# Kernel optimization log

Measured on AMD Instinct MI355X. Metric: run time of the kernel, lower is better.

Reference implementation:

```python
import jax, jax.numpy as jnp
import numpy as np

B, TQ, TP, TC = 8, 8, 447, 1500   # batch, new tokens, past cache len, encoder len
D, H = 1280, 20                   # n_state, n_head
DH = D // H
SCALE = DH ** -0.25               # Whisper scales q and k each by d_head**-0.25
DFF = 4 * D
EPS = 1e-5


def _ln(x, w, b):
    m = jnp.mean(x, axis=-1, keepdims=True)
    v = jnp.mean((x - m) ** 2, axis=-1, keepdims=True)
    return (x - m) * jax.lax.rsqrt(v + EPS) * w + b


def _attn(q, k, v, mask=None):
    # q:[B,Tq,D] k,v:[B,Tk,D]; per-head scaled dot-product attention
    Bq, Tq, _ = q.shape
    Tk = k.shape[1]
    qh = q.reshape(Bq, Tq, H, DH) * SCALE
    kh = k.reshape(Bq, Tk, H, DH) * SCALE
    vh = v.reshape(Bq, Tk, H, DH)
    qk = jnp.einsum('bqhd,bkhd->bhqk', qh, kh)
    if mask is not None:
        qk = qk + mask[None, None, :, :]
    w = jax.nn.softmax(qk, axis=-1)
    return jnp.einsum('bhqk,bkhd->bqhd', w, vh).reshape(Bq, Tq, D)


def setup_inputs() -> dict:
    key = jax.random.key(0)
    ks = jax.random.split(key, 32)
    rn = lambda i, shp, s=1.0: jax.random.normal(ks[i], shp, jnp.float32) * s
    W = 0.02  # weight init scale; weights stored [in,out] so y = x @ W + b
    # additive mask: past fully visible, causal over the TQ new tokens
    i = jnp.arange(TQ)[:, None]
    j = jnp.arange(TQ)[None, :]
    new_mask = jnp.where(j > i, jnp.float32(-1e9), 0.0)
    mask = jnp.concatenate([jnp.zeros((TQ, TP), jnp.float32), new_mask], axis=1)
    return dict(
        x=rn(0, (B, TQ, D)),
        self_k_cache=rn(1, (B, TP, D)),
        self_v_cache=rn(2, (B, TP, D)),
        cross_k=rn(3, (B, TC, D)),
        cross_v=rn(4, (B, TC, D)),
        mask=mask,
        attn_wq=rn(5, (D, D), W), attn_bq=jnp.zeros((D,)),
        attn_wk=rn(6, (D, D), W),                      # Whisper key proj has no bias
        attn_wv=rn(7, (D, D), W), attn_bv=jnp.zeros((D,)),
        attn_wo=rn(8, (D, D), W), attn_bo=jnp.zeros((D,)),
        cross_wq=rn(9, (D, D), W), cross_bq=jnp.zeros((D,)),
        cross_wo=rn(10, (D, D), W), cross_bo=jnp.zeros((D,)),
        attn_ln_w=jnp.ones((D,)), attn_ln_b=jnp.zeros((D,)),
        cross_ln_w=jnp.ones((D,)), cross_ln_b=jnp.zeros((D,)),
        mlp_ln_w=jnp.ones((D,)), mlp_ln_b=jnp.zeros((D,)),
        mlp_w1=rn(11, (D, DFF), W), mlp_b1=jnp.zeros((DFF,)),
        mlp_w2=rn(12, (DFF, D), W), mlp_b2=jnp.zeros((D,)),
        offset=TP,
    )


def reference(x, self_k_cache, self_v_cache, cross_k, cross_v, mask,
              attn_wq, attn_bq, attn_wk, attn_wv, attn_bv, attn_wo, attn_bo,
              cross_wq, cross_bq, cross_wo, cross_bo,
              attn_ln_w, attn_ln_b, cross_ln_w, cross_ln_b, mlp_ln_w, mlp_ln_b,
              mlp_w1, mlp_b1, mlp_w2, mlp_b2, offset):
    # --- self-attention with KV cache ---
    xl = _ln(x, attn_ln_w, attn_ln_b)
    q = xl @ attn_wq + attn_bq
    k1 = xl @ attn_wk
    v1 = xl @ attn_wv + attn_bv
    k = jnp.concatenate([self_k_cache, k1], axis=1)  # [B, TP+TQ, D]
    v = jnp.concatenate([self_v_cache, v1], axis=1)
    x = x + _attn(q, k, v, mask) @ attn_wo + attn_bo
    # --- cross-attention (cross_k/cross_v already projected from encoder) ---
    xl = _ln(x, cross_ln_w, cross_ln_b)
    qc = xl @ cross_wq + cross_bq
    x = x + _attn(qc, cross_k, cross_v) @ cross_wo + cross_bo
    # --- MLP ---
    xl = _ln(x, mlp_ln_w, mlp_ln_b)
    h = jax.nn.gelu(xl @ mlp_w1 + mlp_b1, approximate=False)
    x = x + h @ mlp_w2 + mlp_b2
    return (x, k1, v1)
```

## Files before the change

### kernel.cpp

```cpp
#include <hip/hip_runtime.h>
#include <hip/hip_bf16.h>

#define B_   8
#define TQ_  8
#define TP_  447
#define TC_  1500
#define D_   1280
#define H_   20
#define DH_  64
#define DFF_ 5120
#define M_   64

__global__ __launch_bounds__(256) void ln_kernel(const float* __restrict__ X,
    const float* __restrict__ g, const float* __restrict__ be, float* __restrict__ outT)
{
  __shared__ float redA[4], redB[4];
  const int m = blockIdx.x;
  const int tid = threadIdx.x;
  float v[5];
#pragma unroll
  for (int t = 0; t < 5; ++t) v[t] = X[(size_t)m*D_ + tid + t*256];
  float s = v[0]+v[1]+v[2]+v[3]+v[4];
#pragma unroll
  for (int o = 32; o; o >>= 1) s += __shfl_down(s, o, 64);
  if ((tid & 63) == 0) redA[tid >> 6] = s;
  __syncthreads();
  const float mean = (redA[0]+redA[1]+redA[2]+redA[3]) * (1.0f/D_);
  float q = 0.f;
#pragma unroll
  for (int t = 0; t < 5; ++t) { const float d = v[t]-mean; q += d*d; }
#pragma unroll
  for (int o = 32; o; o >>= 1) q += __shfl_down(q, o, 64);
  if ((tid & 63) == 0) redB[tid >> 6] = q;
  __syncthreads();
  const float rstd = rsqrtf((redB[0]+redB[1]+redB[2]+redB[3]) * (1.0f/D_) + 1e-5f);
#pragma unroll
  for (int t = 0; t < 5; ++t) {
    const int c = tid + t*256;
    outT[(size_t)c*M_ + m] = (v[t]-mean)*rstd*g[c] + be[c];
  }
}

__global__ __launch_bounds__(256) void gemm_splitk(
    const float* __restrict__ XT,
    const float* __restrict__ Wa, const float* __restrict__ Wb, const float* __restrict__ Wc,
    float* __restrict__ Pa, float* __restrict__ Pb, float* __restrict__ Pc,
    int N, int chunk)
{
  __shared__ float xs[64][64];
  __shared__ float wsh[64][128];
  const int z = blockIdx.z;
  const float* W = (z == 0 ? Wa : (z == 1 ? Wb : Wc));
  float* P = (z == 0 ? Pa : (z == 1 ? Pb : Pc));
  const int tid  = threadIdx.x;
  const int lane = tid & 63;
  const int wv   = tid >> 6;
  const int n    = blockIdx.x*128 + lane*2;
  const int k0   = blockIdx.y * chunk;
  float accL[16], accH[16];
#pragma unroll
  for (int r = 0; r < 16; ++r) { accL[r] = 0.f; accH[r] = 0.f; }

  for (int kb = 0; kb < chunk; kb += 64) {
    __syncthreads();
    {
      const float4* src = (const float4*)(XT + (size_t)(k0 + kb)*M_);
      float4* dst = (float4*)&xs[0][0];
#pragma unroll
      for (int i = 0; i < 4; ++i) dst[tid + i*256] = src[tid + i*256];
    }
    {
      const float* Wb0 = W + (size_t)(k0 + kb)*N + blockIdx.x*128;
#pragma unroll
      for (int i = 0; i < 8; ++i) {
        const int idx = tid + i*256;
        const int r = idx >> 5, c = (idx & 31)*4;
        *(float4*)&wsh[r][c] = *(const float4*)(Wb0 + (size_t)r*N + c);
      }
    }
    __syncthreads();
    for (int kk = 0; kk < 64; ++kk) {
      const float2 wp = *(const float2*)&wsh[kk][lane*2];
      const float wl = wp.x;
      const float wh = wp.y;
      const float* xr = &xs[kk][wv*16];
#pragma unroll
      for (int r4 = 0; r4 < 4; ++r4) {
        const float4 xv = *(const float4*)(xr + r4*4);
        accL[r4*4+0] += xv.x*wl; accH[r4*4+0] += xv.x*wh;
        accL[r4*4+1] += xv.y*wl; accH[r4*4+1] += xv.y*wh;
        accL[r4*4+2] += xv.z*wl; accH[r4*4+2] += xv.z*wh;
        accL[r4*4+3] += xv.w*wl; accH[r4*4+3] += xv.w*wh;
      }
    }
  }
#pragma unroll
  for (int r = 0; r < 16; ++r) {
    const int m = wv*16 + r;
    float2 st; st.x = accL[r]; st.y = accH[r];
    *(float2*)(P + ((size_t)blockIdx.y*M_ + m)*N + n) = st;
  }
}

template<int S>
__global__ __launch_bounds__(256) void epilogue_kernel(
    const float* __restrict__ P, int N,
    const float* __restrict__ bias,
    const float* __restrict__ res,
    int gelu,
    float* __restrict__ outA, float* __restrict__ outT, float* __restrict__ outB)
{
  const int idx = blockIdx.x*256 + threadIdx.x;
  const int m = idx / N;
  const int n = idx - m*N;
  float a = 0.f;
#pragma unroll
  for (int s = 0; s < S; ++s) a += P[((size_t)s*M_ + m)*N + n];
  if (bias) a += bias[n];
  if (gelu) a = 0.5f*a*(1.0f + erff(a*0.70710678118654752f));
  if (res) a += res[idx];
  if (outA) outA[idx] = a;
  if (outT) outT[(size_t)n*M_ + m] = a;
  if (outB) outB[idx] = a;
}

template<int S>
__global__ __launch_bounds__(256) void epilogue_ln(
    const float* __restrict__ P,
    const float* __restrict__ bias, const float* __restrict__ res,
    const float* __restrict__ g, const float* __restrict__ be,
    float* __restrict__ outRow, float* __restrict__ outT)
{
  __shared__ float redA[4], redB[4];
  const int m = blockIdx.x;
  const int tid = threadIdx.x;
  float v[5];
#pragma unroll
  for (int t = 0; t < 5; ++t) {
    const int c = tid + t*256;
    float a = 0.f;
#pragma unroll
    for (int s = 0; s < S; ++s) a += P[((size_t)s*M_ + m)*D_ + c];
    a += bias[c] + res[(size_t)m*D_ + c];
    outRow[(size_t)m*D_ + c] = a;
    v[t] = a;
  }
  float s = v[0]+v[1]+v[2]+v[3]+v[4];
#pragma unroll
  for (int o = 32; o; o >>= 1) s += __shfl_down(s, o, 64);
  if ((tid & 63) == 0) redA[tid >> 6] = s;
  __syncthreads();
  const float mean = (redA[0]+redA[1]+redA[2]+redA[3]) * (1.0f/D_);
  float q = 0.f;
#pragma unroll
  for (int t = 0; t < 5; ++t) { const float d = v[t]-mean; q += d*d; }
#pragma unroll
  for (int o = 32; o; o >>= 1) q += __shfl_down(q, o, 64);
  if ((tid & 63) == 0) redB[tid >> 6] = q;
  __syncthreads();
  const float rstd = rsqrtf((redB[0]+redB[1]+redB[2]+redB[3]) * (1.0f/D_) + 1e-5f);
#pragma unroll
  for (int t = 0; t < 5; ++t) {
    const int c = tid + t*256;
    outT[(size_t)c*M_ + m] = (v[t]-mean)*rstd*g[c] + be[c];
  }
}

__global__ __launch_bounds__(256) void epilogue_qkv(
    const float* __restrict__ Pq, const float* __restrict__ Pk, const float* __restrict__ Pv,
    const float* __restrict__ bq, const float* __restrict__ bv,
    float* __restrict__ qbuf, float* __restrict__ k1f, float* __restrict__ v1f,
    float* __restrict__ out_k1, float* __restrict__ out_v1)
{
  const int z = blockIdx.z;
  const int idx = blockIdx.x*256 + threadIdx.x;
  const float* P = (z == 0 ? Pq : (z == 1 ? Pk : Pv));
  float a = 0.f;
#pragma unroll
  for (int s = 0; s < 10; ++s) a += P[(size_t)s*M_*D_ + idx];
  const int n = idx % D_;
  if (z == 0)      { a += bq[n]; qbuf[idx] = a; }
  else if (z == 1) { k1f[idx] = a; out_k1[idx] = a; }
  else             { a += bv[n]; v1f[idx] = a; out_v1[idx] = a; }
}

#define SCS 10
__global__ __launch_bounds__(256, 7) void attn_fused(
    const float* __restrict__ Q,
    const float* __restrict__ Kc, const float* __restrict__ Kn,
    const float* __restrict__ Vc, const float* __restrict__ Vn,
    const float* __restrict__ mask,
    float* __restrict__ Opart, float* __restrict__ ML,
    int TK, int TPp, int chunk)
{
  __shared__ float sc[64*SCS];
  __shared__ float qs[8*64];
  __shared__ float kr[64*68];
  const int tid = threadIdx.x;
  const int sp = blockIdx.x, h = blockIdx.y, b = blockIdx.z;
  const int SP = gridDim.x;
  const int j0 = sp * chunk;
  const int cnt = min(chunk, TK - j0);
  const int bh = b*H_ + h;

  {
    const int i = tid >> 6, d = tid & 63;
    qs[tid]       = Q[((size_t)(b*TQ_ + i    ))*D_ + h*DH_ + d];
    qs[tid + 256] = Q[((size_t)(b*TQ_ + i + 4))*D_ + h*DH_ + d];
  }
  for (int u = tid; u < cnt*16; u += 256) {
    const int r = u >> 4, c = u & 15;
    const int j = j0 + r;
    const float* kg = (j < TPp)
      ? Kc + ((size_t)b*TPp + j)*D_ + h*DH_
      : Kn + ((size_t)(b*TQ_ + (j - TPp)))*D_ + h*DH_;
    *(float4*)&kr[r*68 + c*4] = *(const float4*)(kg + c*4);
  }
  __syncthreads();

  {
    const int jl = tid >> 2, qt = tid & 3;
    if (jl < cnt) {
      const float* krow = &kr[jl*68 + qt*16];
      const float4 k0 = *(const float4*)(krow);
      const float4 k1 = *(const float4*)(krow + 4);
      const float4 k2 = *(const float4*)(krow + 8);
      const float4 k3 = *(const float4*)(krow + 12);
      float acc[8];
#pragma unroll
      for (int i = 0; i < 8; ++i) {
        const float* qp = &qs[i*64 + qt*16];
        const float4 q0 = *(const float4*)(qp);
        const float4 q1 = *(const float4*)(qp + 4);
        const float4 q2 = *(const float4*)(qp + 8);
        const float4 q3 = *(const float4*)(qp + 12);
        acc[i] = q0.x*k0.x + q0.y*k0.y + q0.z*k0.z + q0.w*k0.w
               + q1.x*k1.x + q1.y*k1.y + q1.z*k1.z + q1.w*k1.w
               + q2.x*k2.x + q2.y*k2.y + q2.z*k2.z + q2.w*k2.w
               + q3.x*k3.x + q3.y*k3.y + q3.z*k3.z + q3.w*k3.w;
      }
#pragma unroll
      for (int i = 0; i < 8; ++i) {
        acc[i] += __shfl_xor(acc[i], 1, 64);
        acc[i] += __shfl_xor(acc[i], 2, 64);
      }
      if (qt == 0) {
        const int j = j0 + jl;
#pragma unroll
        for (int i = 0; i < 8; ++i) {
          float vv = acc[i]*0.125f;
          if (mask) vv += mask[(size_t)i*TK + j];
          sc[jl*SCS + i] = vv;
        }
      }
    }
  }
  __syncthreads();

  {
    const int g = tid >> 5, l = tid & 31;
    float mx = -3.0e38f;
    for (int jl = l; jl < cnt; jl += 32) mx = fmaxf(mx, sc[jl*SCS + g]);
#pragma unroll
    for (int o = 16; o; o >>= 1) mx = fmaxf(mx, __shfl_down(mx, o, 32));
    mx = __shfl(mx, 0, 32);
    float sum = 0.f;
    for (int jl = l; jl < cnt; jl += 32) {
      const float e = __expf(sc[jl*SCS + g] - mx);
      sc[jl*SCS + g] = e;
      sum += e;
    }
#pragma unroll
    for (int o = 16; o; o >>= 1) sum += __shfl_down(sum, o, 32);
    if (l == 0) {
      ML[((size_t)bh*SP + sp)*16 + g]     = mx;
      ML[((size_t)bh*SP + sp)*16 + 8 + g] = sum;
    }
  }
  __syncthreads();

  {
    const int wv = tid >> 6;
    const int d  = tid & 63;
    float acc[8] = {0.f,0.f,0.f,0.f,0.f,0.f,0.f,0.f};
#pragma unroll 4
    for (int jl = wv; jl < cnt; jl += 4) {
      const int j = j0 + jl;
      const float vv = (j < TPp)
        ? Vc[((size_t)b*TPp + j)*D_ + h*DH_ + d]
        : Vn[((size_t)(b*TQ_ + (j - TPp)))*D_ + h*DH_ + d];
      const float2 p0 = *(const float2*)&sc[jl*SCS + 0];
      const float2 p1 = *(const float2*)&sc[jl*SCS + 2];
      const float2 p2 = *(const float2*)&sc[jl*SCS + 4];
      const float2 p3 = *(const float2*)&sc[jl*SCS + 6];
      acc[0] += p0.x*vv; acc[1] += p0.y*vv;
      acc[2] += p1.x*vv; acc[3] += p1.y*vv;
      acc[4] += p2.x*vv; acc[5] += p2.y*vv;
      acc[6] += p3.x*vv; acc[7] += p3.y*vv;
    }
#pragma unroll
    for (int i = 0; i < 8; ++i) kr[(wv*8 + i)*64 + d] = acc[i];
  }
  __syncthreads();
  {
#pragma unroll
    for (int t = 0; t < 2; ++t) {
      const int o = tid + t*256;
      const int i = o >> 6, d = o & 63;
      const float r = kr[(0*8 + i)*64 + d] + kr[(1*8 + i)*64 + d]
                    + kr[(2*8 + i)*64 + d] + kr[(3*8 + i)*64 + d];
      Opart[(((size_t)bh*SP + sp)*8 + i)*64 + d] = r;
    }
  }
}

__global__ __launch_bounds__(256) void attn_pv_combine(
    const float* __restrict__ Opart, const float* __restrict__ ML,
    float* __restrict__ outT, int SP)
{
  const int tid = threadIdx.x;
  const int h = blockIdx.x, b = blockIdx.y;
  const int bh = b*H_ + h;
  const int wv = tid >> 6, d = tid & 63;
  const int i0 = wv*2, i1 = i0 + 1;
  float M0 = -3.0e38f, M1 = -3.0e38f;
  for (int s = 0; s < SP; ++s) {
    M0 = fmaxf(M0, ML[((size_t)bh*SP + s)*16 + i0]);
    M1 = fmaxf(M1, ML[((size_t)bh*SP + s)*16 + i1]);
  }
  float L0 = 0.f, L1 = 0.f, o0 = 0.f, o1 = 0.f;
  for (int s = 0; s < SP; ++s) {
    const float w0 = __expf(ML[((size_t)bh*SP + s)*16 + i0] - M0);
    const float w1 = __expf(ML[((size_t)bh*SP + s)*16 + i1] - M1);
    L0 += w0 * ML[((size_t)bh*SP + s)*16 + 8 + i0];
    L1 += w1 * ML[((size_t)bh*SP + s)*16 + 8 + i1];
    o0 += w0 * Opart[(((size_t)bh*SP + s)*8 + i0)*64 + d];
    o1 += w1 * Opart[(((size_t)bh*SP + s)*8 + i1)*64 + d];
  }
  outT[((size_t)(h*DH_ + d))*M_ + b*TQ_ + i0] = o0 / L0;
  outT[((size_t)(h*DH_ + d))*M_ + b*TQ_ + i1] = o1 / L1;
}

extern "C" void kernel_launch(void* const* d_in, const int* in_sizes, int n_in,
                              void* d_out, int out_size, void* d_ws, size_t ws_size,
                              hipStream_t stream)
{
  (void)in_sizes; (void)n_in; (void)out_size; (void)ws_size;
  const float* x    = (const float*)d_in[0];
  const float* skc  = (const float*)d_in[1];
  const float* svc  = (const float*)d_in[2];
  const float* ck   = (const float*)d_in[3];
  const float* cv   = (const float*)d_in[4];
  const float* msk  = (const float*)d_in[5];
  const float* wq   = (const float*)d_in[6];
  const float* bq   = (const float*)d_in[7];
  const float* wk   = (const float*)d_in[8];
  const float* wvv  = (const float*)d_in[9];
  const float* bv   = (const float*)d_in[10];
  const float* wo   = (const float*)d_in[11];
  const float* bo   = (const float*)d_in[12];
  const float* cwq  = (const float*)d_in[13];
  const float* cbq  = (const float*)d_in[14];
  const float* cwo  = (const float*)d_in[15];
  const float* cbo  = (const float*)d_in[16];
  const float* ln1w = (const float*)d_in[17];
  const float* ln1b = (const float*)d_in[18];
  const float* ln2w = (const float*)d_in[19];
  const float* ln2b = (const float*)d_in[20];
  const float* ln3w = (const float*)d_in[21];
  const float* ln3b = (const float*)d_in[22];
  const float* w1   = (const float*)d_in[23];
  const float* b1   = (const float*)d_in[24];
  const float* w2   = (const float*)d_in[25];
  const float* b2   = (const float*)d_in[26];

  float* out_x  = (float*)d_out;
  float* out_k1 = out_x + 81920;
  float* out_v1 = out_x + 163840;

  float* ws = (float*)d_ws;
  float* xlT  = ws + 0;
  float* qbuf = ws + 81920;
  float* k1f  = ws + 163840;
  float* v1f  = ws + 245760;
  float* x2   = ws + 327680;
  float* x3   = ws + 409600;
  float* attT = ws + 491520;
  float* hT   = ws + 573440;
  float* Pg   = ws + 901120;
  float* Pq   = Pg;
  float* Pk   = Pg + 819200;
  float* Pv   = Pg + 1638400;
  float* MLS  = ws + 4177920;
  float* MLC  = ws + 4218880;

  const dim3 blk(256);

  ln_kernel<<<dim3(64), blk, 0, stream>>>(x, ln1w, ln1b, xlT);
  gemm_splitk<<<dim3(10,10,3), blk, 0, stream>>>(xlT, wq, wk, wvv, Pq, Pk, Pv, 1280, 128);
  epilogue_qkv<<<dim3(320,1,3), blk, 0, stream>>>(Pq, Pk, Pv, bq, bv, qbuf, k1f, v1f, out_k1, out_v1);
  attn_fused<<<dim3(8,20,8), blk, 0, stream>>>(qbuf, skc, k1f, svc, v1f, msk, Pg, MLS, 455, 447, 57);
  attn_pv_combine<<<dim3(20,8), blk, 0, stream>>>(Pg, MLS, attT, 8);
  gemm_splitk<<<dim3(10,20,1), blk, 0, stream>>>(attT, wo, wo, wo, Pq, Pq, Pq, 1280, 64);
  epilogue_ln<20><<<dim3(64), blk, 0, stream>>>(Pq, bo, x, ln2w, ln2b, x2, xlT);

  gemm_splitk<<<dim3(10,20,1), blk, 0, stream>>>(xlT, cwq, cwq, cwq, Pq, Pq, Pq, 1280, 64);
  epilogue_kernel<20><<<dim3(320), blk, 0, stream>>>(Pq, 1280, cbq, nullptr, 0, qbuf, nullptr, nullptr);
  attn_fused<<<dim3(24,20,8), blk, 0, stream>>>(qbuf, ck, nullptr, cv, nullptr, nullptr, Pg, MLC, 1500, 1500, 64);
  attn_pv_combine<<<dim3(20,8), blk, 0, stream>>>(Pg, MLC, attT, 24);
  gemm_splitk<<<dim3(10,20,1), blk, 0, stream>>>(attT, cwo, cwo, cwo, Pq, Pq, Pq, 1280, 64);
  epilogue_ln<20><<<dim3(64), blk, 0, stream>>>(Pq, cbo, x2, ln3w, ln3b, x3, xlT);

  gemm_splitk<<<dim3(40,10,1), blk, 0, stream>>>(xlT, w1, w1, w1, Pg, Pg, Pg, 5120, 128);
  epilogue_kernel<10><<<dim3(1280), blk, 0, stream>>>(Pg, 5120, b1, nullptr, 1, nullptr, hT, nullptr);
  gemm_splitk<<<dim3(10,40,1), blk, 0, stream>>>(hT, w2, w2, w2, Pg, Pg, Pg, 1280, 128);
  epilogue_kernel<40><<<dim3(320), blk, 0, stream>>>(Pg, 1280, b2, x3, 0, nullptr, nullptr, out_x);
}
```

Measured before the change: 409.8 us.

## Store GEMM activations row-major and transpose into shared memory during tile load

Activation buffers (layernorm outputs, attention outputs, GELU hidden) are now written row-major with coalesced stores instead of as transposed [K][M] arrays with strided scattered stores. The split-K GEMM takes a leading dimension and transposes each 64x64 A tile into shared memory as it loads it. This removes uncoalesced transposed writes in several producer kernels. In exchange the GEMM's global A loads are strided per row, and the scalar shared-memory stores may hit bank conflicts.

```diff
diff --git a/kernel.cpp b/kernel.cpp
--- a/kernel.cpp
+++ b/kernel.cpp
@@ -12,7 +12,7 @@
 #define M_   64
 
 __global__ __launch_bounds__(256) void ln_kernel(const float* __restrict__ X,
-    const float* __restrict__ g, const float* __restrict__ be, float* __restrict__ outT)
+    const float* __restrict__ g, const float* __restrict__ be, float* __restrict__ out)
 {
   __shared__ float redA[4], redB[4];
   const int m = blockIdx.x;
@@ -37,12 +37,12 @@
 #pragma unroll
   for (int t = 0; t < 5; ++t) {
     const int c = tid + t*256;
-    outT[(size_t)c*M_ + m] = (v[t]-mean)*rstd*g[c] + be[c];
+    out[(size_t)m*D_ + c] = (v[t]-mean)*rstd*g[c] + be[c];
   }
 }
 
 __global__ __launch_bounds__(256) void gemm_splitk(
-    const float* __restrict__ XT,
+    const float* __restrict__ A, int lda,
     const float* __restrict__ Wa, const float* __restrict__ Wb, const float* __restrict__ Wc,
     float* __restrict__ Pa, float* __restrict__ Pb, float* __restrict__ Pc,
     int N, int chunk)
@@ -57,6 +57,8 @@
   const int wv   = tid >> 6;
   const int n    = blockIdx.x*128 + lane*2;
   const int k0   = blockIdx.y * chunk;
+  const int mrow = tid >> 2;
+  const int ks   = (tid & 3) * 16;
   float accL[16], accH[16];
 #pragma unroll
   for (int r = 0; r < 16; ++r) { accL[r] = 0.f; accH[r] = 0.f; }
@@ -64,10 +66,16 @@
   for (int kb = 0; kb < chunk; kb += 64) {
     __syncthreads();
     {
-      const float4* src = (const float4*)(XT + (size_t)(k0 + kb)*M_);
-      float4* dst = (float4*)&xs[0][0];
-#pragma unroll
-      for (int i = 0; i < 4; ++i) dst[tid + i*256] = src[tid + i*256];
+      const float4* arow = (const float4*)(A + (size_t)mrow*lda + k0 + kb + ks);
+#pragma unroll
+      for (int i = 0; i < 4; ++i) {
+        const float4 av = arow[i];
+        const int kk = ks + i*4;
+        xs[kk+0][mrow] = av.x;
+        xs[kk+1][mrow] = av.y;
+        xs[kk+2][mrow] = av.z;
+        xs[kk+3][mrow] = av.w;
+      }
     }
     {
       const float* Wb0 = W + (size_t)(k0 + kb)*N + blockIdx.x*128;
@@ -108,7 +116,7 @@
     const float* __restrict__ bias,
     const float* __restrict__ res,
     int gelu,
-    float* __restrict__ outA, float* __restrict__ outT, float* __restrict__ outB)
+    float* __restrict__ outA, float* __restrict__ outB)
 {
   const int idx = blockIdx.x*256 + threadIdx.x;
   const int m = idx / N;
@@ -120,7 +128,6 @@
   if (gelu) a = 0.5f*a*(1.0f + erff(a*0.70710678118654752f));
   if (res) a += res[idx];
   if (outA) outA[idx] = a;
-  if (outT) outT[(size_t)n*M_ + m] = a;
   if (outB) outB[idx] = a;
 }
 
@@ -129,7 +136,7 @@
     const float* __restrict__ P,
     const float* __restrict__ bias, const float* __restrict__ res,
     const float* __restrict__ g, const float* __restrict__ be,
-    float* __restrict__ outRow, float* __restrict__ outT)
+    float* __restrict__ outRow, float* __restrict__ outLN)
 {
   __shared__ float redA[4], redB[4];
   const int m = blockIdx.x;
@@ -162,7 +169,7 @@
 #pragma unroll
   for (int t = 0; t < 5; ++t) {
     const int c = tid + t*256;
-    outT[(size_t)c*M_ + m] = (v[t]-mean)*rstd*g[c] + be[c];
+    outLN[(size_t)m*D_ + c] = (v[t]-mean)*rstd*g[c] + be[c];
   }
 }
 
@@ -316,7 +323,7 @@
 
 __global__ __launch_bounds__(256) void attn_pv_combine(
     const float* __restrict__ Opart, const float* __restrict__ ML,
-    float* __restrict__ outT, int SP)
+    float* __restrict__ out, int SP)
 {
   const int tid = threadIdx.x;
   const int h = blockIdx.x, b = blockIdx.y;
@@ -337,8 +344,8 @@
     o0 += w0 * Opart[(((size_t)bh*SP + s)*8 + i0)*64 + d];
     o1 += w1 * Opart[(((size_t)bh*SP + s)*8 + i1)*64 + d];
   }
-  outT[((size_t)(h*DH_ + d))*M_ + b*TQ_ + i0] = o0 / L0;
-  outT[((size_t)(h*DH_ + d))*M_ + b*TQ_ + i1] = o1 / L1;
+  out[((size_t)(b*TQ_ + i0))*D_ + h*DH_ + d] = o0 / L0;
+  out[((size_t)(b*TQ_ + i1))*D_ + h*DH_ + d] = o1 / L1;
 }
 
 extern "C" void kernel_launch(void* const* d_in, const int* in_sizes, int n_in,
@@ -379,14 +386,14 @@
   float* out_v1 = out_x + 163840;
 
   float* ws = (float*)d_ws;
-  float* xlT  = ws + 0;
+  float* xl   = ws + 0;
   float* qbuf = ws + 81920;
   float* k1f  = ws + 163840;
   float* v1f  = ws + 245760;
   float* x2   = ws + 327680;
   float* x3   = ws + 409600;
-  float* attT = ws + 491520;
-  float* hT   = ws + 573440;
+  float* attO = ws + 491520;
+  float* hbuf = ws + 573440;
   float* Pg   = ws + 901120;
   float* Pq   = Pg;
   float* Pk   = Pg + 819200;
@@ -396,23 +403,23 @@
 
   const dim3 blk(256);
 
-  ln_kernel<<<dim3(64), blk, 0, stream>>>(x, ln1w, ln1b, xlT);
-  gemm_splitk<<<dim3(10,10,3), blk, 0, stream>>>(xlT, wq, wk, wvv, Pq, Pk, Pv, 1280, 128);
+  ln_kernel<<<dim3(64), blk, 0, stream>>>(x, ln1w, ln1b, xl);
+  gemm_splitk<<<dim3(10,10,3), blk, 0, stream>>>(xl, D_, wq, wk, wvv, Pq, Pk, Pv, 1280, 128);
   epilogue_qkv<<<dim3(320,1,3), blk, 0, stream>>>(Pq, Pk, Pv, bq, bv, qbuf, k1f, v1f, out_k1, out_v1);
   attn_fused<<<dim3(8,20,8), blk, 0, stream>>>(qbuf, skc, k1f, svc, v1f, msk, Pg, MLS, 455, 447, 57);
-  attn_pv_combine<<<dim3(20,8), blk, 0, stream>>>(Pg, MLS, attT, 8);
-  gemm_splitk<<<dim3(10,20,1), blk, 0, stream>>>(attT, wo, wo, wo, Pq, Pq, Pq, 1280, 64);
-  epilogue_ln<20><<<dim3(64), blk, 0, stream>>>(Pq, bo, x, ln2w, ln2b, x2, xlT);
-
-  gemm_splitk<<<dim3(10,20,1), blk, 0, stream>>>(xlT, cwq, cwq, cwq, Pq, Pq, Pq, 1280, 64);
-  epilogue_kernel<20><<<dim3(320), blk, 0, stream>>>(Pq, 1280, cbq, nullptr, 0, qbuf, nullptr, nullptr);
+  attn_pv_combine<<<dim3(20,8), blk, 0, stream>>>(Pg, MLS, attO, 8);
+  gemm_splitk<<<dim3(10,20,1), blk, 0, stream>>>(attO, D_, wo, wo, wo, Pq, Pq, Pq, 1280, 64);
+  epilogue_ln<20><<<dim3(64), blk, 0, stream>>>(Pq, bo, x, ln2w, ln2b, x2, xl);
+
+  gemm_splitk<<<dim3(10,20,1), blk, 0, stream>>>(xl, D_, cwq, cwq, cwq, Pq, Pq, Pq, 1280, 64);
+  epilogue_kernel<20><<<dim3(320), blk, 0, stream>>>(Pq, 1280, cbq, nullptr, 0, qbuf, nullptr);
   attn_fused<<<dim3(24,20,8), blk, 0, stream>>>(qbuf, ck, nullptr, cv, nullptr, nullptr, Pg, MLC, 1500, 1500, 64);
-  attn_pv_combine<<<dim3(20,8), blk, 0, stream>>>(Pg, MLC, attT, 24);
-  gemm_splitk<<<dim3(10,20,1), blk, 0, stream>>>(attT, cwo, cwo, cwo, Pq, Pq, Pq, 1280, 64);
-  epilogue_ln<20><<<dim3(64), blk, 0, stream>>>(Pq, cbo, x2, ln3w, ln3b, x3, xlT);
-
-  gemm_splitk<<<dim3(40,10,1), blk, 0, stream>>>(xlT, w1, w1, w1, Pg, Pg, Pg, 5120, 128);
-  epilogue_kernel<10><<<dim3(1280), blk, 0, stream>>>(Pg, 5120, b1, nullptr, 1, nullptr, hT, nullptr);
-  gemm_splitk<<<dim3(10,40,1), blk, 0, stream>>>(hT, w2, w2, w2, Pg, Pg, Pg, 1280, 128);
-  epilogue_kernel<40><<<dim3(320), blk, 0, stream>>>(Pg, 1280, b2, x3, 0, nullptr, nullptr, out_x);
-}
+  attn_pv_combine<<<dim3(20,8), blk, 0, stream>>>(Pg, MLC, attO, 24);
+  gemm_splitk<<<dim3(10,20,1), blk, 0, stream>>>(attO, D_, cwo, cwo, cwo, Pq, Pq, Pq, 1280, 64);
+  epilogue_ln<20><<<dim3(64), blk, 0, stream>>>(Pq, cbo, x2, ln3w, ln3b, x3, xl);
+
+  gemm_splitk<<<dim3(40,10,1), blk, 0, stream>>>(xl, D_, w1, w1, w1, Pg, Pg, Pg, 5120, 128);
+  epilogue_kernel<10><<<dim3(1280), blk, 0, stream>>>(Pg, 5120, b1, nullptr, 1, hbuf, nullptr);
+  gemm_splitk<<<dim3(10,40,1), blk, 0, stream>>>(hbuf, DFF_, w2, w2, w2, Pg, Pg, Pg, 1280, 128);
+  epilogue_kernel<40><<<dim3(320), blk, 0, stream>>>(Pg, 1280, b2, x3, 0, out_x, nullptr);
+}
```

After: 400.6 us. 1.02x faster.
